# Performance work log

Hardware: AMD Instinct MI355X
Metric: run time of the kernel (lower is better)

## Reference

```python
import jax, jax.numpy as jnp
import numpy as np

D_MODEL = 1024
NUM_HEADS = 16
MAX_SEQ_LEN = 2048
THETA = 10000.0
HEAD_DIM = D_MODEL // NUM_HEADS  # 64


def _trunc_normal(key, shape, std):
    # truncated normal in [-3, 3] sigma, matching nn.init.trunc_normal_
    return std * jax.random.truncated_normal(key, -3.0, 3.0, shape, dtype=jnp.float32)


def setup_inputs() -> dict:
    key = jax.random.key(0)
    kx, kq, kk, kv, ko = jax.random.split(key, 5)
    B, L = 2, 2048
    sigma = np.sqrt(2.0 / (D_MODEL + D_MODEL))
    x = jax.random.normal(kx, (B, L, D_MODEL), dtype=jnp.float32)
    token_positions = jnp.arange(L, dtype=jnp.int64 if jax.config.jax_enable_x64 else jnp.int32)[None, :]
    return {
        "x": x,
        "wq": _trunc_normal(kq, (D_MODEL, D_MODEL), sigma),
        "wk": _trunc_normal(kk, (D_MODEL, D_MODEL), sigma),
        "wv": _trunc_normal(kv, (D_MODEL, D_MODEL), sigma),
        "wo": _trunc_normal(ko, (D_MODEL, D_MODEL), sigma),
        "token_positions": token_positions,
    }


def _rope_tables():
    pos = jnp.arange(MAX_SEQ_LEN, dtype=jnp.float32)
    d_idx = jnp.arange(HEAD_DIM // 2, dtype=jnp.float32)
    inv_freq = THETA ** (-2.0 * d_idx / HEAD_DIM)
    angles = pos[:, None] * inv_freq[None, :]  # [max_seq_len, head_dim/2]
    return jnp.cos(angles), jnp.sin(angles)


def _apply_rope(x, cos, sin):
    # x: [b, n, l, h]; cos/sin: [1, l, h/2] (broadcast over b, n)
    xe = x[..., 0::2]
    xo = x[..., 1::2]
    oe = cos * xe - sin * xo
    oo = sin * xe + cos * xo
    # interleave back: stack last axis then flatten pairs
    out = jnp.stack([oe, oo], axis=-1)
    return out.reshape(x.shape)


def reference(x, wq, wk, wv, wo, token_positions):
    B, L, _ = x.shape
    cos_t, sin_t = _rope_tables()
    cos = cos_t[token_positions]  # [1, L, h/2]
    sin = sin_t[token_positions]

    def proj(w):
        y = jnp.einsum('bld,ed->ble', x, w)
        return y.reshape(B, L, NUM_HEADS, HEAD_DIM).transpose(0, 2, 1, 3)  # b n l h

    q, k, v = proj(wq), proj(wk), proj(wv)
    q = _apply_rope(q, cos, sin)
    k = _apply_rope(k, cos, sin)

    scale = 1.0 / np.sqrt(HEAD_DIM).astype(np.float32)
    logits = jnp.einsum('bnqh,bnkh->bnqk', q, k) * scale
    causal = jnp.tril(jnp.ones((L, L), dtype=bool))
    logits = jnp.where(causal[None, None], logits, -jnp.inf)
    scores = jax.nn.softmax(logits, axis=-1)
    out = jnp.einsum('bnqk,bnkh->bnqh', scores, v)
    out = out.transpose(0, 2, 1, 3).reshape(B, L, D_MODEL)
    return jnp.einsum('bld,ed->ble', out, wo)
```

## Files before the change

### kernel.cpp

```cpp
#include <hip/hip_runtime.h>
#include <stdint.h>
#include <stddef.h>

#define SEQ   2048
#define HD    64
#define DM    1024
#define NHEAD 16

typedef __bf16 bf16x8 __attribute__((ext_vector_type(8)));
typedef __bf16 bf16x4 __attribute__((ext_vector_type(4)));
typedef float  f32x4  __attribute__((ext_vector_type(4)));
typedef uint32_t u32x2 __attribute__((ext_vector_type(2)));
typedef uint32_t u32x4 __attribute__((ext_vector_type(4)));

#define MFMA16x16(a, b, c) __builtin_amdgcn_mfma_f32_16x16x32_bf16((a), (b), (c), 0, 0, 0)

__device__ __forceinline__ void gload16(const void* g, void* lds_uniform) {
    __builtin_amdgcn_global_load_lds(
        (const __attribute__((address_space(1))) uint32_t*)g,
        (__attribute__((address_space(3))) uint32_t*)lds_uniform, 16, 0, 0);
}

__global__ void prep_kernel(const float* __restrict__ x,
                            const float* __restrict__ wq, const float* __restrict__ wk,
                            const float* __restrict__ wv, const float* __restrict__ wo,
                            __bf16* __restrict__ xb, __bf16* __restrict__ wqkv,
                            __bf16* __restrict__ wob, float2* __restrict__ ctst) {
    int bid = blockIdx.x;
    if (bid < 4096) {
        int i = (bid * 256 + threadIdx.x) * 4;
        const float4 v = *(const float4*)(x + i);
        __bf16 o[4] = {(__bf16)v.x, (__bf16)v.y, (__bf16)v.z, (__bf16)v.w};
        *(uint64_t*)(xb + i) = *(const uint64_t*)o;
    } else if (bid < 8192) {
        int g = (bid - 4096) >> 10;
        int i = (((bid - 4096) & 1023) * 256 + threadIdx.x) * 4;
        const float* src = (g == 0) ? wq : (g == 1) ? wk : (g == 2) ? wv : wo;
        __bf16* dst = (g == 3) ? wob : (wqkv + (size_t)g * 1048576);
        const float4 v = *(const float4*)(src + i);
        __bf16 o[4] = {(__bf16)v.x, (__bf16)v.y, (__bf16)v.z, (__bf16)v.w};
        *(uint64_t*)(dst + i) = *(const uint64_t*)o;
    } else {
        int i = (bid - 8192) * 256 + threadIdx.x;
        int p = i & 31;
        int pos = i >> 5;
        float freq = expf(-(float)p * (logf(10000.0f) / 32.0f));
        float ang = (float)pos * freq;
        ctst[i] = make_float2(cosf(ang), sinf(ang));
    }
}

template <int MODE, int BN>
__global__ __launch_bounds__(256, 4)
void gemm_bt_kernel(const __bf16* __restrict__ A, const __bf16* __restrict__ W,
                    float* __restrict__ C, __bf16* __restrict__ Qb,
                    __bf16* __restrict__ Kb, __bf16* __restrict__ VTb,
                    const int* __restrict__ tpos, const float2* __restrict__ ctst,
                    int N, int K) {
    constexpr int NJ = BN >> 5;
    __shared__ __align__(16) char smem[16384 + BN * 128];
    char* As = smem;
    char* Bs = smem + 16384;
    const int lane = threadIdx.x & 63;
    const int w    = threadIdx.x >> 6;

    const int nbn = N / BN;
    const int per = (nbn * 32) >> 3;
    const int id  = blockIdx.x;
    const int lin = (id & 7) * per + (id >> 3);
    const int bm  = lin / nbn;
    const int bn  = lin % nbn;

    const int rbase = (w >> 1) * 64;
    const int cbase = (w & 1) * (BN / 2);

    f32x4 acc[4][NJ] = {};

    const int kt_iters = K >> 6;
    for (int kt = 0; kt < kt_iters; ++kt) {
        #pragma unroll
        for (int c = 0; c < 4; ++c) {
            int id2 = (c * 4 + w) * 64 + lane;
            int row = id2 >> 3, cc = id2 & 7;
            int koff = kt * 64 + ((cc ^ (row & 7)) << 3);
            gload16(A + (size_t)(bm * 128 + row) * K + koff, As + (c * 4 + w) * 1024);
        }
        #pragma unroll
        for (int c = 0; c < NJ; ++c) {
            int id2 = (c * 4 + w) * 64 + lane;
            int row = id2 >> 3, cc = id2 & 7;
            int koff = kt * 64 + ((cc ^ (row & 7)) << 3);
            gload16(W + (size_t)(bn * BN + row) * K + koff, Bs + (c * 4 + w) * 1024);
        }
        __syncthreads();
        #pragma unroll
        for (int ks = 0; ks < 2; ++ks) {
            bf16x8 af[4], bfr[NJ];
            #pragma unroll
            for (int i = 0; i < 4; ++i) {
                int row = rbase + i * 16 + (lane & 15);
                int c = ks * 4 + (lane >> 4);
                af[i] = *(const bf16x8*)(As + row * 128 + ((c ^ (row & 7)) << 4));
            }
            #pragma unroll
            for (int j = 0; j < NJ; ++j) {
                int row = cbase + j * 16 + (lane & 15);
                int c = ks * 4 + (lane >> 4);
                bfr[j] = *(const bf16x8*)(Bs + row * 128 + ((c ^ (row & 7)) << 4));
            }
            #pragma unroll
            for (int i = 0; i < 4; ++i)
                #pragma unroll
                for (int j = 0; j < NJ; ++j)
                    acc[i][j] = MFMA16x16(af[i], bfr[j], acc[i][j]);
        }
        __syncthreads();
    }

    if (MODE == 1) {
        #pragma unroll
        for (int i = 0; i < 4; ++i)
            #pragma unroll
            for (int j = 0; j < NJ; ++j)
                #pragma unroll
                for (int r = 0; r < 4; ++r) {
                    int m = bm * 128 + rbase + i * 16 + (lane >> 4) * 4 + r;
                    int n = bn * BN + cbase + j * 16 + (lane & 15);
                    C[(size_t)m * N + n] = acc[i][j][r];
                }
    } else {
        const int which = bn >> 3;
        char* T = smem + w * 8192;
        #pragma unroll
        for (int i = 0; i < 4; ++i)
            #pragma unroll
            for (int j = 0; j < NJ; ++j)
                #pragma unroll
                for (int r = 0; r < 4; ++r) {
                    int mi = i * 16 + (lane >> 4) * 4 + r;
                    int ni = j * 16 + (lane & 15);
                    __bf16 v = (__bf16)acc[i][j][r];
                    if (which == 2)
                        *(__bf16*)(T + ni * 128 + ((mi * 2) ^ ((ni & 7) << 4))) = v;
                    else
                        *(__bf16*)(T + mi * 128 + ((ni * 2) ^ ((mi & 7) << 4))) = v;
                }
        #pragma unroll
        for (int it = 0; it < 8; ++it) {
            int id2 = it * 64 + lane;
            int row = id2 >> 3, cc = id2 & 7;
            bf16x8 v = *(const bf16x8*)(T + row * 128 + ((cc ^ (row & 7)) << 4));
            if (which == 2) {
                int n = bn * BN + cbase + row;
                int m = bm * 128 + rbase + cc * 8;
                int b = m >> 11, l = m & (SEQ - 1);
                int h = (n & (DM - 1)) >> 6, d = n & 63;
                *(bf16x8*)(VTb + ((size_t)((b * NHEAD + h) * HD + d) * SEQ) + l) = v;
            } else {
                int m = bm * 128 + rbase + row;
                int n = bn * BN + cbase + cc * 8;
                int b = m >> 11, l = m & (SEQ - 1);
                int h = (n & (DM - 1)) >> 6, d = n & 63;
                int pb = tpos[l] * 32 + (d >> 1);
                float sc = (which == 0) ? 0.18033688011112042f : 1.0f;
                bf16x8 ov;
                #pragma unroll
                for (int jj = 0; jj < 4; ++jj) {
                    float2 cs = ctst[pb + jj];
                    float e = (float)v[2 * jj], dd = (float)v[2 * jj + 1];
                    ov[2 * jj]     = (__bf16)(sc * (cs.x * e - cs.y * dd));
                    ov[2 * jj + 1] = (__bf16)(sc * (cs.y * e + cs.x * dd));
                }
                __bf16* dst = which ? Kb : Qb;
                *(bf16x8*)(dst + ((size_t)(b * NHEAD + h) * SEQ + l) * HD + d) = ov;
            }
        }
    }
}

__global__ __launch_bounds__(256, 4)
void attn_kernel(const __bf16* __restrict__ Q, const __bf16* __restrict__ K,
                 const __bf16* __restrict__ VT, __bf16* __restrict__ O) {
    __shared__ __align__(16) char smem[32768];
    const int lane = threadIdx.x & 63;
    const int w    = threadIdx.x >> 6;
    const int tid  = threadIdx.x;
    const int hi   = lane >> 4;
    const int lo   = lane & 15;

    const int bid = blockIdx.x;
    const int xcd = bid & 7;
    const int idx = bid >> 3;
    const int s   = idx & 31;
    const int r   = idx >> 5;
    const int bh  = xcd * 4 + r;
    const int qb  = (r & 1) ? s : (31 - s);

    const __bf16* Qbh  = Q  + (size_t)bh * SEQ * HD;
    const __bf16* Kbh  = K  + (size_t)bh * SEQ * HD;
    const __bf16* VTbh = VT + (size_t)bh * HD * SEQ;
    const int b = bh >> 4, h = bh & 15;

    {
        #pragma unroll
        for (int c = 0; c < 2; ++c) {
            int id = c * 256 + tid;
            int row = id >> 3, cc = id & 7;
            int sw = (cc ^ (row & 7)) << 3;
            gload16(Kbh + (size_t)row * HD + sw, smem + (c * 4 + w) * 1024);
        }
        #pragma unroll
        for (int c = 0; c < 2; ++c) {
            int id = c * 256 + tid;
            int row = id >> 3, cc = id & 7;
            int jA = ((cc >> 2) << 5) | ((cc & 3) << 2);
            u32x2 a = *(const u32x2*)(VTbh + (size_t)row * SEQ + jA);
            u32x2 bq = *(const u32x2*)(VTbh + (size_t)row * SEQ + jA + 16);
            u32x4 v4 = {a[0], a[1], bq[0], bq[1]};
            *(u32x4*)(smem + 8192 + row * 128 + ((cc ^ (row & 7)) << 4)) = v4;
        }
    }

    const int qrow = qb * 64 + w * 16 + lo;
    bf16x8 qf[2];
    qf[0] = *(const bf16x8*)(Qbh + (size_t)qrow * HD + hi * 8);
    qf[1] = *(const bf16x8*)(Qbh + (size_t)qrow * HD + 32 + hi * 8);

    bf16x8 ones;
    #pragma unroll
    for (int i = 0; i < 8; ++i) ones[i] = (__bf16)1.0f;

    f32x4 o[4] = {};
    f32x4 ls = {};

    int cur = 0;
    __syncthreads();

    for (int kb = 0; kb <= qb; ++kb) {
        bf16x8 kreg[2];
        u32x4  vreg[2];
        if (kb < qb) {
            #pragma unroll
            for (int c = 0; c < 2; ++c) {
                int id = c * 256 + tid;
                int row = id >> 3, cc = id & 7;
                kreg[c] = *(const bf16x8*)(Kbh + (size_t)((kb + 1) * 64 + row) * HD + cc * 8);
                int jA = ((cc >> 2) << 5) | ((cc & 3) << 2);
                const __bf16* vsrc = VTbh + (size_t)row * SEQ + (kb + 1) * 64 + jA;
                u32x2 a = *(const u32x2*)(vsrc);
                u32x2 bq = *(const u32x2*)(vsrc + 16);
                vreg[c] = u32x4{a[0], a[1], bq[0], bq[1]};
            }
        }

        char* Ks = smem + cur * 16384;
        char* Vs = Ks + 8192;

        f32x4 s4[4];
        __builtin_amdgcn_s_setprio(1);
        #pragma unroll
        for (int jt = 0; jt < 4; ++jt) {
            f32x4 z = {};
            #pragma unroll
            for (int ks = 0; ks < 2; ++ks) {
                int row = jt * 16 + lo;
                int c = ks * 4 + hi;
                bf16x8 kf = *(const bf16x8*)(Ks + row * 128 + ((c ^ (row & 7)) << 4));
                z = MFMA16x16(kf, qf[ks], z);
            }
            s4[jt] = z;
        }
        __builtin_amdgcn_s_setprio(0);

        if (kb == qb) {
            int i = qb * 64 + w * 16 + lo;
            #pragma unroll
            for (int jt = 0; jt < 4; ++jt)
                #pragma unroll
                for (int rr = 0; rr < 4; ++rr) {
                    int j = kb * 64 + jt * 16 + hi * 4 + rr;
                    if (j > i) s4[jt][rr] = -1e30f;
                }
        }

        bf16x8 pk8[2];
        #pragma unroll
        for (int js = 0; js < 2; ++js)
            #pragma unroll
            for (int e = 0; e < 8; ++e)
                pk8[js][e] = (__bf16)exp2f(s4[2 * js + (e >> 2)][e & 3] - 16.0f);

        __builtin_amdgcn_s_setprio(1);
        #pragma unroll
        for (int js = 0; js < 2; ++js) {
            ls = MFMA16x16(pk8[js], ones, ls);
            int cb = js * 4 + hi;
            #pragma unroll
            for (int dt = 0; dt < 4; ++dt) {
                int vrow = dt * 16 + lo;
                bf16x8 vf = *(const bf16x8*)(Vs + vrow * 128 + ((cb ^ (vrow & 7)) << 4));
                o[dt] = MFMA16x16(pk8[js], vf, o[dt]);
            }
        }
        __builtin_amdgcn_s_setprio(0);

        if (kb < qb) {
            char* Kn = smem + (cur ^ 1) * 16384;
            char* Vn = Kn + 8192;
            #pragma unroll
            for (int c = 0; c < 2; ++c) {
                int id = c * 256 + tid;
                int row = id >> 3, cc = id & 7;
                int sw = (cc ^ (row & 7)) << 4;
                *(bf16x8*)(Kn + row * 128 + sw) = kreg[c];
                *(u32x4*)(Vn + row * 128 + sw) = vreg[c];
            }
        }

        __syncthreads();
        cur ^= 1;
    }

    float linv[4];
    #pragma unroll
    for (int rr = 0; rr < 4; ++rr) linv[rr] = 1.0f / ls[rr];

    char* Os = smem;
    #pragma unroll
    for (int dt = 0; dt < 4; ++dt)
        #pragma unroll
        for (int rr = 0; rr < 4; ++rr) {
            int orow = w * 16 + hi * 4 + rr;
            int oc = (dt * 16 + lo) * 2;
            *(__bf16*)(Os + orow * 128 + (oc ^ ((orow & 7) << 4))) = (__bf16)(o[dt][rr] * linv[rr]);
        }
    __syncthreads();

    #pragma unroll
    for (int c = 0; c < 2; ++c) {
        int id = c * 256 + tid;
        int row = id >> 3, cc = id & 7;
        bf16x8 v = *(const bf16x8*)(Os + row * 128 + ((cc ^ (row & 7)) << 4));
        *(bf16x8*)(O + (size_t)(b * SEQ + qb * 64 + row) * DM + h * HD + cc * 8) = v;
    }
}

extern "C" void kernel_launch(void* const* d_in, const int* in_sizes, int n_in,
                              void* d_out, int out_size, void* d_ws, size_t ws_size,
                              hipStream_t stream) {
    const float* x  = (const float*)d_in[0];
    const float* wq = (const float*)d_in[1];
    const float* wk = (const float*)d_in[2];
    const float* wv = (const float*)d_in[3];
    const float* wo = (const float*)d_in[4];
    const int* tpos = (const int*)d_in[5];
    float* out = (float*)d_out;
    char* ws = (char*)d_ws;

    __bf16* xb   = (__bf16*)(ws);
    __bf16* wqkv = (__bf16*)(ws + (size_t)(8  << 20));
    __bf16* wob  = (__bf16*)(ws + (size_t)(14 << 20));
    __bf16* Qb   = (__bf16*)(ws + (size_t)(16 << 20));
    __bf16* Kb   = (__bf16*)(ws + (size_t)(24 << 20));
    __bf16* VTb  = (__bf16*)(ws + (size_t)(32 << 20));
    __bf16* Ob   = (__bf16*)(ws + (size_t)(40 << 20));
    float2* ctst = (float2*)(ws + (size_t)(48 << 20));

    prep_kernel<<<8448, 256, 0, stream>>>(x, wq, wk, wv, wo, xb, wqkv, wob, ctst);
    gemm_bt_kernel<0, 128><<<768, 256, 0, stream>>>(xb, wqkv, nullptr, Qb, Kb, VTb,
                                                    tpos, ctst, 3072, 1024);
    attn_kernel<<<1024, 256, 0, stream>>>(Qb, Kb, VTb, Ob);
    gemm_bt_kernel<1, 32><<<1024, 256, 0, stream>>>(Ob, wob, out, nullptr, nullptr, nullptr,
                                                    nullptr, nullptr, 1024, 1024);
}
```

Measured before the change: 99.42 us.

## Peel diagonal attention block, skip masked tiles, retune GEMM tiles and occupancy

The attention loop now handles only the fully visible key blocks, and the diagonal block is peeled into a separate epilogue. In that epilogue each wave skips the QK^T MFMAs for key sub-tiles entirely above its rows, and the PV pass runs only as many slices as the wave needs. This drops the per-iteration branch checks and some wasted causal work. Separately, the QKV GEMM launch bound drops from 4 to 3 waves per EU, and the output GEMM moves from BN=32 with 1024 blocks to BN=64 with 512 blocks, which trades parallelism for data reuse.

```diff
diff --git a/kernel.cpp b/kernel.cpp
--- a/kernel.cpp
+++ b/kernel.cpp
@@ -50,8 +50,8 @@
     }
 }
 
-template <int MODE, int BN>
-__global__ __launch_bounds__(256, 4)
+template <int MODE, int BN, int WPEU>
+__global__ __launch_bounds__(256, WPEU)
 void gemm_bt_kernel(const __bf16* __restrict__ A, const __bf16* __restrict__ W,
                     float* __restrict__ C, __bf16* __restrict__ Qb,
                     __bf16* __restrict__ Kb, __bf16* __restrict__ VTb,
@@ -236,21 +236,19 @@
     int cur = 0;
     __syncthreads();
 
-    for (int kb = 0; kb <= qb; ++kb) {
+    for (int kb = 0; kb < qb; ++kb) {
         bf16x8 kreg[2];
         u32x4  vreg[2];
-        if (kb < qb) {
-            #pragma unroll
-            for (int c = 0; c < 2; ++c) {
-                int id = c * 256 + tid;
-                int row = id >> 3, cc = id & 7;
-                kreg[c] = *(const bf16x8*)(Kbh + (size_t)((kb + 1) * 64 + row) * HD + cc * 8);
-                int jA = ((cc >> 2) << 5) | ((cc & 3) << 2);
-                const __bf16* vsrc = VTbh + (size_t)row * SEQ + (kb + 1) * 64 + jA;
-                u32x2 a = *(const u32x2*)(vsrc);
-                u32x2 bq = *(const u32x2*)(vsrc + 16);
-                vreg[c] = u32x4{a[0], a[1], bq[0], bq[1]};
-            }
+        #pragma unroll
+        for (int c = 0; c < 2; ++c) {
+            int id = c * 256 + tid;
+            int row = id >> 3, cc = id & 7;
+            kreg[c] = *(const bf16x8*)(Kbh + (size_t)((kb + 1) * 64 + row) * HD + cc * 8);
+            int jA = ((cc >> 2) << 5) | ((cc & 3) << 2);
+            const __bf16* vsrc = VTbh + (size_t)row * SEQ + (kb + 1) * 64 + jA;
+            u32x2 a = *(const u32x2*)(vsrc);
+            u32x2 bq = *(const u32x2*)(vsrc + 16);
+            vreg[c] = u32x4{a[0], a[1], bq[0], bq[1]};
         }
 
         char* Ks = smem + cur * 16384;
@@ -272,17 +270,6 @@
         }
         __builtin_amdgcn_s_setprio(0);
 
-        if (kb == qb) {
-            int i = qb * 64 + w * 16 + lo;
-            #pragma unroll
-            for (int jt = 0; jt < 4; ++jt)
-                #pragma unroll
-                for (int rr = 0; rr < 4; ++rr) {
-                    int j = kb * 64 + jt * 16 + hi * 4 + rr;
-                    if (j > i) s4[jt][rr] = -1e30f;
-                }
-        }
-
         bf16x8 pk8[2];
         #pragma unroll
         for (int js = 0; js < 2; ++js)
@@ -304,7 +291,7 @@
         }
         __builtin_amdgcn_s_setprio(0);
 
-        if (kb < qb) {
+        {
             char* Kn = smem + (cur ^ 1) * 16384;
             char* Vn = Kn + 8192;
             #pragma unroll
@@ -320,6 +307,62 @@
         __syncthreads();
         cur ^= 1;
     }
+
+    {
+        char* Ks = smem + cur * 16384;
+        char* Vs = Ks + 8192;
+
+        f32x4 s4[4];
+        __builtin_amdgcn_s_setprio(1);
+        #pragma unroll
+        for (int jt = 0; jt < 4; ++jt) {
+            if (jt <= w) {
+                f32x4 z = {};
+                #pragma unroll
+                for (int ks = 0; ks < 2; ++ks) {
+                    int row = jt * 16 + lo;
+                    int c = ks * 4 + hi;
+                    bf16x8 kf = *(const bf16x8*)(Ks + row * 128 + ((c ^ (row & 7)) << 4));
+                    z = MFMA16x16(kf, qf[ks], z);
+                }
+                s4[jt] = z;
+            } else {
+                s4[jt] = f32x4{-1e30f, -1e30f, -1e30f, -1e30f};
+            }
+        }
+        __builtin_amdgcn_s_setprio(0);
+
+        {
+            int i16 = w * 16 + lo;
+            #pragma unroll
+            for (int jt = 0; jt < 4; ++jt)
+                #pragma unroll
+                for (int rr = 0; rr < 4; ++rr)
+                    if (jt * 16 + hi * 4 + rr > i16) s4[jt][rr] = -1e30f;
+        }
+
+        bf16x8 pk8[2];
+        #pragma unroll
+        for (int js = 0; js < 2; ++js)
+            #pragma unroll
+            for (int e = 0; e < 8; ++e)
+                pk8[js][e] = (__bf16)exp2f(s4[2 * js + (e >> 2)][e & 3] - 16.0f);
+
+        const int njs = (w >> 1) + 1;
+        __builtin_amdgcn_s_setprio(1);
+        for (int js = 0; js < njs; ++js) {
+            ls = MFMA16x16(pk8[js], ones, ls);
+            int cb = js * 4 + hi;
+            #pragma unroll
+            for (int dt = 0; dt < 4; ++dt) {
+                int vrow = dt * 16 + lo;
+                bf16x8 vf = *(const bf16x8*)(Vs + vrow * 128 + ((cb ^ (vrow & 7)) << 4));
+                o[dt] = MFMA16x16(pk8[js], vf, o[dt]);
+            }
+        }
+        __builtin_amdgcn_s_setprio(0);
+    }
+    __syncthreads();
 
     float linv[4];
     #pragma unroll
@@ -367,9 +410,9 @@
     float2* ctst = (float2*)(ws + (size_t)(48 << 20));
 
     prep_kernel<<<8448, 256, 0, stream>>>(x, wq, wk, wv, wo, xb, wqkv, wob, ctst);
-    gemm_bt_kernel<0, 128><<<768, 256, 0, stream>>>(xb, wqkv, nullptr, Qb, Kb, VTb,
-                                                    tpos, ctst, 3072, 1024);
+    gemm_bt_kernel<0, 128, 3><<<768, 256, 0, stream>>>(xb, wqkv, nullptr, Qb, Kb, VTb,
+                                                       tpos, ctst, 3072, 1024);
     attn_kernel<<<1024, 256, 0, stream>>>(Qb, Kb, VTb, Ob);
-    gemm_bt_kernel<1, 32><<<1024, 256, 0, stream>>>(Ob, wob, out, nullptr, nullptr, nullptr,
-                                                    nullptr, nullptr, 1024, 1024);
+    gemm_bt_kernel<1, 64, 4><<<512, 256, 0, stream>>>(Ob, wob, out, nullptr, nullptr, nullptr,
+                                                      nullptr, nullptr, 1024, 1024);
 }
```

Measured after the change: 102.2 us. 2.8% more time.
